# Performance work log

Measured on AMD Instinct MI355X. Metric: run time of the kernel, lower is better.

## Reference

```python
import jax, jax.numpy as jnp
import numpy as np

# Architecture constants (from init_kwargs)
IN_DIM, D_MODEL, HEADDIM, D_STATE, EXPAND, OUT_DIM = 57, 64, 32, 32, 2, 6
D_INNER = EXPAND * D_MODEL          # 128
NHEADS = D_INNER // HEADDIM         # 4
D_CONV = 4                          # causal depthwise conv width (mamba default)
D_XBC = D_INNER + 2 * D_STATE       # 192 (x, B, C share the conv)
D_IN_PROJ = 2 * D_INNER + 2 * D_STATE + NHEADS  # z, xBC, dt -> 324
BATCH, SEQ = 16, 2048


def setup_inputs() -> dict:
    key = jax.random.key(0)
    ks = jax.random.split(key, 12)
    s = 0.02
    return {
        "x": jax.random.normal(ks[0], (BATCH, SEQ, IN_DIM), jnp.float32),
        "W_lin": jax.random.normal(ks[1], (IN_DIM, D_MODEL), jnp.float32) * s,
        "b_lin": jnp.zeros((D_MODEL,), jnp.float32),
        "W_in": jax.random.normal(ks[2], (D_MODEL, D_IN_PROJ), jnp.float32) * s,
        "conv_w": jax.random.normal(ks[3], (D_XBC, 1, D_CONV), jnp.float32) * 0.5,
        "conv_b": jnp.zeros((D_XBC,), jnp.float32),
        "dt_bias": jnp.log(jax.random.uniform(ks[4], (NHEADS,), jnp.float32, 0.001, 0.1)),
        "A_log": jnp.log(jnp.arange(1, NHEADS + 1, dtype=jnp.float32)),
        "D": jnp.ones((NHEADS,), jnp.float32),
        "norm_w": jnp.ones((D_INNER,), jnp.float32),
        "W_out": jax.random.normal(ks[5], (D_INNER, D_MODEL), jnp.float32) * s,
        "W_cls": jax.random.normal(ks[6], (D_MODEL, OUT_DIM), jnp.float32) * s,
        "b_cls": jnp.zeros((OUT_DIM,), jnp.float32),
    }


def _mamba_block(h, W_in, conv_w, conv_b, dt_bias, A_log, D, norm_w, W_out):
    B, L, _ = h.shape
    zxbcdt = h @ W_in                                   # [B,L,324]
    z = zxbcdt[..., :D_INNER]                           # gate [B,L,128]
    xBC = zxbcdt[..., D_INNER:D_INNER + D_XBC]          # [B,L,192]
    dt = zxbcdt[..., D_INNER + D_XBC:]                  # [B,L,H]

    # causal depthwise conv over time + silu
    xBC = jax.lax.conv_general_dilated(
        xBC.transpose(0, 2, 1), conv_w, (1,), [(D_CONV - 1, 0)],
        dimension_numbers=("NCH", "OIH", "NCH"), feature_group_count=D_XBC)
    xBC = jax.nn.silu(xBC + conv_b[None, :, None]).transpose(0, 2, 1)

    xs = xBC[..., :D_INNER].reshape(B, L, NHEADS, HEADDIM)   # [B,L,H,P]
    Bm = xBC[..., D_INNER:D_INNER + D_STATE]                 # [B,L,N]
    Cm = xBC[..., D_INNER + D_STATE:]                        # [B,L,N]

    dt = jax.nn.softplus(dt + dt_bias)                       # [B,L,H]
    A = -jnp.exp(A_log)                                      # [H]

    def step(hstate, t):
        dtt, xt, bt, ct = t                                  # [B,H],[B,H,P],[B,N],[B,N]
        decay = jnp.exp(dtt * A)[:, :, None, None]           # [B,H,1,1]
        hstate = hstate * decay + (dtt[:, :, None] * xt)[..., None] * bt[:, None, None, :]
        y = jnp.einsum("bhpn,bn->bhp", hstate, ct)
        return hstate, y

    h0 = jnp.zeros((B, NHEADS, HEADDIM, D_STATE), h.dtype)
    _, ys = jax.lax.scan(step, h0, (dt.transpose(1, 0, 2), xs.transpose(1, 0, 2, 3),
                                    Bm.transpose(1, 0, 2), Cm.transpose(1, 0, 2)))
    y = ys.transpose(1, 0, 2, 3) + D[None, None, :, None] * xs   # [B,L,H,P]
    y = y.reshape(B, L, D_INNER)

    # gated RMSNorm + out proj
    y = y * jax.nn.silu(z)
    y = y * jax.lax.rsqrt(jnp.mean(y * y, axis=-1, keepdims=True) + 1e-5) * norm_w
    return y @ W_out                                        # [B,L,D_MODEL]


def reference(x, W_lin, b_lin, W_in, conv_w, conv_b, dt_bias, A_log, D, norm_w,
              W_out, W_cls, b_cls):
    h = x @ W_lin + b_lin                                   # linear_in
    h = _mamba_block(h, W_in, conv_w, conv_b, dt_bias, A_log, D, norm_w, W_out)
    pooled = h.mean(axis=1)                                 # AdaptiveAvgPool1d(1)
    return pooled @ W_cls + b_cls                           # classifier [B,6]
```

## Files before the change

kernel.cpp:

```cpp
#include <hip/hip_runtime.h>
#include <hip/hip_fp16.h>
#include <cmath>

#define BATCH   16
#define SEQ     2048
#define IN_DIM  57
#define D_MODEL 64
#define HEADDIM 32
#define D_STATE 32
#define OUT_DIM 6
#define D_INNER 128
#define NHEADS  4
#define D_CONV  4
#define D_XBC   192
#define D_IN_PROJ 324
#define BL      (BATCH*SEQ)

#define NCHUNK  64
#define CLEN    (SEQ / NCHUNK)
#define SUBL    16
#define XDS     200

#define OFF_WF   ((size_t)0)
#define OFF_BF   ((size_t)18496)
#define OFF_WOC  ((size_t)18848)
#define OFF_P    ((size_t)21792)
#define OFF_DC   ((size_t)25920)
#define OFF_ZB   ((size_t)157000)
#define OFF_CB   (OFF_ZB + (size_t)BL*64)
#define OFF_YB   (OFF_CB + (size_t)BL*16)
#define OFF_SB   (OFF_YB + (size_t)BL*64)

__global__ void fuse_w_kernel(const float* __restrict__ W_lin,
                              const float* __restrict__ b_lin,
                              const float* __restrict__ W_in,
                              const float* __restrict__ W_out,
                              const float* __restrict__ W_cls,
                              float* __restrict__ Wf, float* __restrict__ bf,
                              float* __restrict__ Woc,
                              const float* __restrict__ b_cls,
                              float* __restrict__ out) {
    int idx = blockIdx.x * 256 + threadIdx.x;
    if (idx < BATCH * OUT_DIM) out[idx] = b_cls[idx % OUT_DIM];
    if (idx < 58 * D_IN_PROJ) {
        int r = idx / D_IN_PROJ;
        int j = idx - r * D_IN_PROJ;
        const float* v = (r < IN_DIM) ? (W_lin + r * D_MODEL) : b_lin;
        float acc = 0.f;
#pragma unroll 8
        for (int m = 0; m < D_MODEL; ++m) acc += v[m] * W_in[m * D_IN_PROJ + j];
        if (r < IN_DIM) Wf[r * D_IN_PROJ + j] = acc;
        else            bf[j] = acc;
    } else if (idx < 58 * D_IN_PROJ + D_INNER * OUT_DIM) {
        int idx2 = idx - 58 * D_IN_PROJ;
        int i = idx2 / OUT_DIM;
        int o = idx2 - i * OUT_DIM;
        float acc = 0.f;
#pragma unroll 8
        for (int j = 0; j < D_MODEL; ++j)
            acc += W_out[i * D_MODEL + j] * W_cls[j * OUT_DIM + o];
        Woc[i * OUT_DIM + o] = acc;
    }
}

__global__ __launch_bounds__(256) void mega1_kernel(
        const float* __restrict__ x,
        const float* __restrict__ Wf, const float* __restrict__ bf,
        const float* __restrict__ conv_w, const float* __restrict__ conv_b,
        const float* __restrict__ dt_bias, const float* __restrict__ A_log,
        const float* __restrict__ Dp,
        __half* __restrict__ zbh,
        __half* __restrict__ sbuf, float* __restrict__ Pbuf,
        __half* __restrict__ ybuf, __half* __restrict__ Cbuf,
        float* __restrict__ Dcum) {
    __shared__ __align__(16) char smem[40112];
    float (*xs)[60]    = (float (*)[60])smem;
    float (*xbt)[D_XBC]= (float (*)[D_XBC])smem;
    __half (*xdl)[XDS] = (__half (*)[XDS])(smem + 24576);
    __half (*yl)[D_INNER] = (__half (*)[D_INNER])(smem + 24576);
    float (*ddl)[8]    = (float (*)[8])(smem + 38576);
    float* dcl         = (float*)(smem + 39600);

    int b = blockIdx.x >> 6;
    int c = blockIdx.x & (NCHUNK - 1);
    int tid = threadIdx.x;
    long rbase = (long)b * SEQ + (long)c * CLEN;

    for (int i = tid; i < 35 * IN_DIM; i += 256) {
        int r = i / IN_DIM, k = i - r * IN_DIM;
        float v = 0.f;
        if (c > 0 || r >= 3) v = x[(rbase - 3 + r) * IN_DIM + k];
        xs[r][k] = v;
    }
    __syncthreads();

    if (tid < 245) {
        int rset = tid / 49, cg = tid - rset * 49;
        int j0 = 128 + cg * 4;
        float4 bias = *(const float4*)(bf + j0);
        float4 acc[7];
#pragma unroll
        for (int r = 0; r < 7; ++r) acc[r] = bias;
        const float* w = Wf + j0;
        const float* xrow = &xs[rset * 7][0];
#pragma unroll 2
        for (int kc = 0; kc < 14; ++kc) {
            int k = kc * 4;
            float4 wv0 = *(const float4*)(w + (size_t)(k + 0) * D_IN_PROJ);
            float4 wv1 = *(const float4*)(w + (size_t)(k + 1) * D_IN_PROJ);
            float4 wv2 = *(const float4*)(w + (size_t)(k + 2) * D_IN_PROJ);
            float4 wv3 = *(const float4*)(w + (size_t)(k + 3) * D_IN_PROJ);
#pragma unroll
            for (int r = 0; r < 7; ++r) {
                float4 xv = *(const float4*)(xrow + r * 60 + k);
                acc[r].x += xv.x * wv0.x + xv.y * wv1.x + xv.z * wv2.x + xv.w * wv3.x;
                acc[r].y += xv.x * wv0.y + xv.y * wv1.y + xv.z * wv2.y + xv.w * wv3.y;
                acc[r].z += xv.x * wv0.z + xv.y * wv1.z + xv.z * wv2.z + xv.w * wv3.z;
                acc[r].w += xv.x * wv0.w + xv.y * wv1.w + xv.z * wv2.w + xv.w * wv3.w;
            }
        }
        {
            float4 wv = *(const float4*)(w + (size_t)56 * D_IN_PROJ);
#pragma unroll
            for (int r = 0; r < 7; ++r) {
                float xv = xrow[r * 60 + 56];
                acc[r].x += xv * wv.x; acc[r].y += xv * wv.y;
                acc[r].z += xv * wv.z; acc[r].w += xv * wv.w;
            }
        }
#pragma unroll
        for (int r = 0; r < 7; ++r) {
            int row = rset * 7 + r;
            *(__half2*)&xdl[row][j0 - 128]     = __floats2half2_rn(acc[r].x, acc[r].y);
            *(__half2*)&xdl[row][j0 - 128 + 2] = __floats2half2_rn(acc[r].z, acc[r].w);
        }
    }

    {
        int rset = tid >> 5, cg = tid & 31;
        int j0 = cg * 4;
        float4 bias = *(const float4*)(bf + j0);
        float4 acc[4];
#pragma unroll
        for (int r = 0; r < 4; ++r) acc[r] = bias;
        const float* w = Wf + j0;
        const float* xrow = &xs[3 + rset * 4][0];
#pragma unroll 2
        for (int kc = 0; kc < 14; ++kc) {
            int k = kc * 4;
            float4 wv0 = *(const float4*)(w + (size_t)(k + 0) * D_IN_PROJ);
            float4 wv1 = *(const float4*)(w + (size_t)(k + 1) * D_IN_PROJ);
            float4 wv2 = *(const float4*)(w + (size_t)(k + 2) * D_IN_PROJ);
            float4 wv3 = *(const float4*)(w + (size_t)(k + 3) * D_IN_PROJ);
#pragma unroll
            for (int r = 0; r < 4; ++r) {
                float4 xv = *(const float4*)(xrow + r * 60 + k);
                acc[r].x += xv.x * wv0.x + xv.y * wv1.x + xv.z * wv2.x + xv.w * wv3.x;
                acc[r].y += xv.x * wv0.y + xv.y * wv1.y + xv.z * wv2.y + xv.w * wv3.y;
                acc[r].z += xv.x * wv0.z + xv.y * wv1.z + xv.z * wv2.z + xv.w * wv3.z;
                acc[r].w += xv.x * wv0.w + xv.y * wv1.w + xv.z * wv2.w + xv.w * wv3.w;
            }
        }
        {
            float4 wv = *(const float4*)(w + (size_t)56 * D_IN_PROJ);
#pragma unroll
            for (int r = 0; r < 4; ++r) {
                float xv = xrow[r * 60 + 56];
                acc[r].x += xv * wv.x; acc[r].y += xv * wv.y;
                acc[r].z += xv * wv.z; acc[r].w += xv * wv.w;
            }
        }
#pragma unroll
        for (int r = 0; r < 4; ++r) {
            long row = rbase + rset * 4 + r;
            __half2 h01 = __floats2half2_rn(acc[r].x, acc[r].y);
            __half2 h23 = __floats2half2_rn(acc[r].z, acc[r].w);
            uint2 u;
            u.x = *(unsigned*)&h01;
            u.y = *(unsigned*)&h23;
            *(uint2*)(zbh + row * D_INNER + j0) = u;
        }
    }
    __syncthreads();

    if (tid < D_XBC) {
        int ch = tid;
        float w0 = conv_w[ch*4+0], w1 = conv_w[ch*4+1];
        float w2 = conv_w[ch*4+2], w3 = conv_w[ch*4+3];
        float cb = conv_b[ch];
        float vm1 = 0.f, vm2 = 0.f, vm3 = 0.f;
        if (c > 0) {
            vm1 = __half2float(xdl[2][ch]);
            vm2 = __half2float(xdl[1][ch]);
            vm3 = __half2float(xdl[0][ch]);
        }
#pragma unroll
        for (int i = 0; i < CLEN; ++i) {
            float v0 = __half2float(xdl[i + 3][ch]);
            float a = cb + v0 * w3 + vm1 * w2 + vm2 * w1 + vm3 * w0;
            xbt[i][ch] = a / (1.f + expf(-a));
            vm3 = vm2; vm2 = vm1; vm1 = v0;
        }
    } else {
        int idx = tid - D_XBC;
        int h = idx >> 4;
        int i0 = idx & 15;
        float db = dt_bias[h];
        float nA = -expf(A_log[h]);
#pragma unroll
        for (int i = i0; i < CLEN; i += 16) {
            float v = __half2float(xdl[i + 3][192 + h]) + db;
            float dtv = (v > 20.f) ? v : log1pf(expf(v));
            ddl[i][h * 2]     = dtv;
            ddl[i][h * 2 + 1] = expf(dtv * nA);
        }
    }
    __syncthreads();

    int h = tid >> 6, lane = tid & 63;
    int p = lane >> 1, n0 = (lane & 1) * 16;
    float Dh = Dp[h];
    float4 s0 = make_float4(0.f,0.f,0.f,0.f), s1 = s0, s2 = s0, s3 = s0;
    float pacc = 1.f;
#pragma unroll 4
    for (int i = 0; i < CLEN; ++i) {
        float dtv = ddl[i][h * 2];
        float dec = ddl[i][h * 2 + 1];
        float xv = xbt[i][h * HEADDIM + p];
        const float* Bp = &xbt[i][D_INNER + n0];
        const float* Cp = &xbt[i][D_INNER + D_STATE + n0];
        float4 B0 = *(const float4*)(Bp + 0);
        float4 B1 = *(const float4*)(Bp + 4);
        float4 B2 = *(const float4*)(Bp + 8);
        float4 B3 = *(const float4*)(Bp + 12);
        float4 C0 = *(const float4*)(Cp + 0);
        float4 C1 = *(const float4*)(Cp + 4);
        float4 C2 = *(const float4*)(Cp + 8);
        float4 C3 = *(const float4*)(Cp + 12);
        float coef = dtv * xv;
        s0.x = s0.x*dec + coef*B0.x; s0.y = s0.y*dec + coef*B0.y;
        s0.z = s0.z*dec + coef*B0.z; s0.w = s0.w*dec + coef*B0.w;
        s1.x = s1.x*dec + coef*B1.x; s1.y = s1.y*dec + coef*B1.y;
        s1.z = s1.z*dec + coef*B1.z; s1.w = s1.w*dec + coef*B1.w;
        s2.x = s2.x*dec + coef*B2.x; s2.y = s2.y*dec + coef*B2.y;
        s2.z = s2.z*dec + coef*B2.z; s2.w = s2.w*dec + coef*B2.w;
        s3.x = s3.x*dec + coef*B3.x; s3.y = s3.y*dec + coef*B3.y;
        s3.z = s3.z*dec + coef*B3.z; s3.w = s3.w*dec + coef*B3.w;
        pacc *= dec;
        float part = s0.x*C0.x + s0.y*C0.y + s0.z*C0.z + s0.w*C0.w
                   + s1.x*C1.x + s1.y*C1.y + s1.z*C1.z + s1.w*C1.w
                   + s2.x*C2.x + s2.y*C2.y + s2.z*C2.z + s2.w*C2.w
                   + s3.x*C3.x + s3.y*C3.y + s3.z*C3.z + s3.w*C3.w;
        part += __shfl_xor(part, 1);
        if (lane == 0) dcl[i * 4 + h] = pacc;
        if ((lane & 1) == 0)
            yl[i][h * HEADDIM + p] = __float2half(part + Dh * xv);
    }
    int bh = b * NHEADS + h;
    __half2 hs[8];
    hs[0] = __floats2half2_rn(s0.x, s0.y); hs[1] = __floats2half2_rn(s0.z, s0.w);
    hs[2] = __floats2half2_rn(s1.x, s1.y); hs[3] = __floats2half2_rn(s1.z, s1.w);
    hs[4] = __floats2half2_rn(s2.x, s2.y); hs[5] = __floats2half2_rn(s2.z, s2.w);
    hs[6] = __floats2half2_rn(s3.x, s3.y); hs[7] = __floats2half2_rn(s3.z, s3.w);
    uint4* sp = (uint4*)(sbuf + ((size_t)bh * NCHUNK + c) * 1024) + lane * 2;
    sp[0] = *(uint4*)&hs[0];
    sp[1] = *(uint4*)&hs[4];
    if (lane == 0) Pbuf[bh * NCHUNK + c] = pacc;
    __syncthreads();
    {
        const uint4* ysrc = (const uint4*)&yl[0][0];
        uint4* ydst = (uint4*)(ybuf + (size_t)rbase * D_INNER);
        ydst[tid]       = ysrc[tid];
        ydst[tid + 256] = ysrc[tid + 256];
    }
    for (int idx = tid; idx < CLEN * 16; idx += 256) {
        int r  = idx >> 4;
        int n2 = (idx & 15) * 2;
        __half2 hv = __floats2half2_rn(xbt[r][D_INNER + D_STATE + n2],
                                       xbt[r][D_INNER + D_STATE + n2 + 1]);
        *((__half2*)(Cbuf + ((size_t)rbase + r) * D_STATE + n2)) = hv;
    }
    if (tid < CLEN * 4) Dcum[(size_t)rbase * 4 + tid] = dcl[tid];
}

__global__ __launch_bounds__(256) void scan_phase2_kernel(
        __half* __restrict__ sbuf, const float* __restrict__ Pbuf) {
    __shared__ unsigned sl[NCHUNK][128];
    __shared__ float Pl[NCHUNK];
    int bh = blockIdx.x >> 2;
    int q  = blockIdx.x & 3;
    int tid = threadIdx.x;
    unsigned* s32 = (unsigned*)sbuf;
    size_t base = (size_t)bh * NCHUNK * 512 + (size_t)q * 128;
    if (tid < NCHUNK) Pl[tid] = Pbuf[bh * NCHUNK + tid];
    for (int k = tid; k < NCHUNK * 128; k += 256) {
        int c = k >> 7, j = k & 127;
        sl[c][j] = s32[base + (size_t)c * 512 + j];
    }
    __syncthreads();
    if (tid < 128) {
        float rx = 0.f, ry = 0.f;
        unsigned v = sl[0][tid];
#pragma unroll 8
        for (int c = 0; c < NCHUNK; ++c) {
            unsigned vn = (c + 1 < NCHUNK) ? sl[c + 1][tid] : 0u;
            float Pv = Pl[c];
            __half2 hv = *(__half2*)&v;
            float2 t = __half22float2(hv);
            __half2 hr = __floats2half2_rn(rx, ry);
            sl[c][tid] = *(unsigned*)&hr;
            rx = rx * Pv + t.x;
            ry = ry * Pv + t.y;
            v = vn;
        }
    }
    __syncthreads();
    for (int k = tid; k < NCHUNK * 128; k += 256) {
        int c = k >> 7, j = k & 127;
        s32[base + (size_t)c * 512 + j] = sl[c][j];
    }
}

__global__ __launch_bounds__(256) void scan_phase3_kernel(
        const __half* __restrict__ ybuf, const __half* __restrict__ Cbuf,
        const float* __restrict__ Dcum, const __half* __restrict__ zbh,
        const __half* __restrict__ sbuf, const float* __restrict__ norm_w,
        const float* __restrict__ Woc, float* __restrict__ out) {
    int b  = blockIdx.x >> 7;
    int sc = blockIdx.x & 127;
    int c  = sc >> 1;
    int tid = threadIdx.x;
    __shared__ float ylds[SUBL][D_INNER];
    __shared__ float dcl[SUBL * 4];
    __shared__ float red[4][D_INNER];
    __shared__ float snw[D_INNER];
    size_t rbase = (size_t)b * SEQ + (size_t)sc * SUBL;
    int h = tid >> 6, lane = tid & 63;
    int p = lane >> 1, n0 = (lane & 1) * 16;
    int bh = b * NHEADS + h;
    const uint4* sp = (const uint4*)(sbuf + ((size_t)bh * NCHUNK + c) * 1024) + lane * 2;
    uint4 u0 = sp[0], u1 = sp[1];
    {
        const __half2* ysrc = (const __half2*)(ybuf + rbase * D_INNER);
#pragma unroll
        for (int k = 0; k < 4; ++k) {
            int idx = tid + k * 256;
            float2 f = __half22float2(ysrc[idx]);
            int r  = idx >> 6;
            int c2 = (idx & 63) * 2;
            ylds[r][c2]     = f.x;
            ylds[r][c2 + 1] = f.y;
        }
    }
    if (tid < SUBL * 4) dcl[tid] = Dcum[rbase * 4 + tid];
    float4 s0, s1, s2, s3;
    {
        const __half2* hp0 = (const __half2*)&u0;
        const __half2* hp1 = (const __half2*)&u1;
        float2 f;
        f = __half22float2(hp0[0]); s0.x = f.x; s0.y = f.y;
        f = __half22float2(hp0[1]); s0.z = f.x; s0.w = f.y;
        f = __half22float2(hp0[2]); s1.x = f.x; s1.y = f.y;
        f = __half22float2(hp0[3]); s1.z = f.x; s1.w = f.y;
        f = __half22float2(hp1[0]); s2.x = f.x; s2.y = f.y;
        f = __half22float2(hp1[1]); s2.z = f.x; s2.w = f.y;
        f = __half22float2(hp1[2]); s3.x = f.x; s3.y = f.y;
        f = __half22float2(hp1[3]); s3.z = f.x; s3.w = f.y;
    }
    __syncthreads();
#pragma unroll 4
    for (int i = 0; i < SUBL; ++i) {
        const uint4* cp = (const uint4*)(Cbuf + (rbase + i) * D_STATE + n0);
        uint4 ca = cp[0], cb = cp[1];
        const __half2* cha = (const __half2*)&ca;
        const __half2* chb = (const __half2*)&cb;
        float2 f0 = __half22float2(cha[0]);
        float2 f1 = __half22float2(cha[1]);
        float2 f2 = __half22float2(cha[2]);
        float2 f3 = __half22float2(cha[3]);
        float2 f4 = __half22float2(chb[0]);
        float2 f5 = __half22float2(chb[1]);
        float2 f6 = __half22float2(chb[2]);
        float2 f7 = __half22float2(chb[3]);
        float part = s0.x*f0.x + s0.y*f0.y + s0.z*f1.x + s0.w*f1.y
                   + s1.x*f2.x + s1.y*f2.y + s1.z*f3.x + s1.w*f3.y
                   + s2.x*f4.x + s2.y*f4.y + s2.z*f5.x + s2.w*f5.y
                   + s3.x*f6.x + s3.y*f6.y + s3.z*f7.x + s3.w*f7.y;
        part += __shfl_xor(part, 1);
        if ((lane & 1) == 0)
            ylds[i][h * HEADDIM + p] += dcl[i * 4 + h] * part;
    }
    __syncthreads();
    float acc0 = 0.f, acc1 = 0.f;
    for (int r = h; r < SUBL; r += 4) {
        size_t bl = rbase + r;
        float2 yv = *(const float2*)(&ylds[r][lane * 2]);
        float2 zv = __half22float2(*((const __half2*)(zbh + bl * D_INNER) + lane));
        float g0 = yv.x * (zv.x / (1.f + expf(-zv.x)));
        float g1 = yv.y * (zv.y / (1.f + expf(-zv.y)));
        float sq = g0 * g0 + g1 * g1;
#pragma unroll
        for (int m = 1; m < 64; m <<= 1) sq += __shfl_xor(sq, m);
        float rms = 1.0f / sqrtf(sq * (1.f / 128.f) + 1e-5f);
        acc0 += g0 * rms;
        acc1 += g1 * rms;
    }
    red[h][lane * 2]     = acc0;
    red[h][lane * 2 + 1] = acc1;
    __syncthreads();
    if (tid < D_INNER)
        snw[tid] = (red[0][tid] + red[1][tid] + red[2][tid] + red[3][tid])
                   * norm_w[tid];
    __syncthreads();
    if (tid < OUT_DIM) {
        float acc = 0.f;
#pragma unroll 8
        for (int i = 0; i < D_INNER; ++i)
            acc += snw[i] * Woc[i * OUT_DIM + tid];
        atomicAdd(&out[b * OUT_DIM + tid], acc * (1.f / (float)SEQ));
    }
}

extern "C" void kernel_launch(void* const* d_in, const int* in_sizes, int n_in,
                              void* d_out, int out_size, void* d_ws, size_t ws_size,
                              hipStream_t stream) {
    const float* x       = (const float*)d_in[0];
    const float* W_lin   = (const float*)d_in[1];
    const float* b_lin   = (const float*)d_in[2];
    const float* W_in    = (const float*)d_in[3];
    const float* conv_w  = (const float*)d_in[4];
    const float* conv_b  = (const float*)d_in[5];
    const float* dt_bias = (const float*)d_in[6];
    const float* A_log   = (const float*)d_in[7];
    const float* Dp      = (const float*)d_in[8];
    const float* norm_w  = (const float*)d_in[9];
    const float* W_out   = (const float*)d_in[10];
    const float* W_cls   = (const float*)d_in[11];
    const float* b_cls   = (const float*)d_in[12];
    float* out = (float*)d_out;

    float* ws = (float*)d_ws;
    float* Wf    = ws + OFF_WF;
    float* bf    = ws + OFF_BF;
    float* Woc   = ws + OFF_WOC;
    float* Pbuf  = ws + OFF_P;
    float* Dcum  = ws + OFF_DC;
    __half* zbh  = (__half*)(ws + OFF_ZB);
    __half* Cbh  = (__half*)(ws + OFF_CB);
    __half* ybh  = (__half*)(ws + OFF_YB);
    __half* sbuf = (__half*)(ws + OFF_SB);

    fuse_w_kernel<<<(58 * D_IN_PROJ + D_INNER * OUT_DIM + 255) / 256, 256, 0, stream>>>(
        W_lin, b_lin, W_in, W_out, W_cls, Wf, bf, Woc, b_cls, out);

    mega1_kernel<<<BATCH * NCHUNK, 256, 0, stream>>>(
        x, Wf, bf, conv_w, conv_b, dt_bias, A_log, Dp,
        zbh, sbuf, Pbuf, ybh, Cbh, Dcum);

    scan_phase2_kernel<<<256, 256, 0, stream>>>(sbuf, Pbuf);

    scan_phase3_kernel<<<BATCH * 128, 256, 0, stream>>>(
        ybh, Cbh, Dcum, zbh, sbuf, norm_w, Woc, out);
}
```

Measured before the change: 168.1 us.

## Compute fused input projection with fp16 MFMA and pre-packed weights

Replaces the scalar FP32 fused linear_in+in_proj GEMM in the main kernel with MFMA 16x16x32 fp16 instructions. Weights are pre-packed in the prep kernel into an MFMA-friendly fp16 layout, and inputs are staged in LDS as XOR-swizzled fp16. The z-gate output now goes through LDS and is written out with coalesced 16-byte stores. This trades FP32 input precision for fp16 operands, which could affect accuracy.

Result: faster. 150.4 us (-10.6%).

```diff
diff --git a/kernel.cpp b/kernel.cpp
--- a/kernel.cpp
+++ b/kernel.cpp
@@ -21,12 +21,18 @@
 #define SUBL    16
 #define XDS     200
 
-#define OFF_WF   ((size_t)0)
-#define OFF_BF   ((size_t)18496)
-#define OFF_WOC  ((size_t)18848)
-#define OFF_P    ((size_t)21792)
-#define OFF_DC   ((size_t)25920)
-#define OFF_ZB   ((size_t)157000)
+#define NT      21
+#define WP_HALFS (NT * 2 * 64 * 8)
+
+typedef _Float16 f16x8 __attribute__((ext_vector_type(8)));
+typedef float    f32x4 __attribute__((ext_vector_type(4)));
+
+#define OFF_WP   ((size_t)0)
+#define OFF_BF   ((size_t)10752)
+#define OFF_WOC  ((size_t)11088)
+#define OFF_P    ((size_t)11856)
+#define OFF_DC   ((size_t)15952)
+#define OFF_ZB   ((size_t)147024)
 #define OFF_CB   (OFF_ZB + (size_t)BL*64)
 #define OFF_YB   (OFF_CB + (size_t)BL*16)
 #define OFF_SB   (OFF_YB + (size_t)BL*64)
@@ -36,23 +42,33 @@
                               const float* __restrict__ W_in,
                               const float* __restrict__ W_out,
                               const float* __restrict__ W_cls,
-                              float* __restrict__ Wf, float* __restrict__ bf,
+                              __half* __restrict__ Wph, float* __restrict__ bf,
                               float* __restrict__ Woc,
                               const float* __restrict__ b_cls,
                               float* __restrict__ out) {
     int idx = blockIdx.x * 256 + threadIdx.x;
-    if (idx < BATCH * OUT_DIM) out[idx] = b_cls[idx % OUT_DIM];
-    if (idx < 58 * D_IN_PROJ) {
-        int r = idx / D_IN_PROJ;
-        int j = idx - r * D_IN_PROJ;
-        const float* v = (r < IN_DIM) ? (W_lin + r * D_MODEL) : b_lin;
+    if (idx < 64 * 336) {
+        int k = idx / 336;
+        int n = idx - k * 336;
+        float acc = 0.f;
+        if (k < IN_DIM && n < D_IN_PROJ) {
+#pragma unroll 8
+            for (int m = 0; m < D_MODEL; ++m)
+                acc += W_lin[k * D_MODEL + m] * W_in[m * D_IN_PROJ + n];
+        }
+        int t = n >> 4, nl = n & 15;
+        int kb = k >> 5, kr = k & 31;
+        size_t pidx = (((size_t)(t * 2 + kb) * 64) + (kr >> 3) * 16 + nl) * 8 + (kr & 7);
+        Wph[pidx] = __float2half(acc);
+    } else if (idx < 64 * 336 + D_IN_PROJ) {
+        int n = idx - 64 * 336;
         float acc = 0.f;
 #pragma unroll 8
-        for (int m = 0; m < D_MODEL; ++m) acc += v[m] * W_in[m * D_IN_PROJ + j];
-        if (r < IN_DIM) Wf[r * D_IN_PROJ + j] = acc;
-        else            bf[j] = acc;
-    } else if (idx < 58 * D_IN_PROJ + D_INNER * OUT_DIM) {
-        int idx2 = idx - 58 * D_IN_PROJ;
+        for (int m = 0; m < D_MODEL; ++m)
+            acc += b_lin[m] * W_in[m * D_IN_PROJ + n];
+        bf[n] = acc;
+    } else if (idx < 64 * 336 + D_IN_PROJ + D_INNER * OUT_DIM) {
+        int idx2 = idx - (64 * 336 + D_IN_PROJ);
         int i = idx2 / OUT_DIM;
         int o = idx2 - i * OUT_DIM;
         float acc = 0.f;
@@ -60,12 +76,15 @@
         for (int j = 0; j < D_MODEL; ++j)
             acc += W_out[i * D_MODEL + j] * W_cls[j * OUT_DIM + o];
         Woc[i * OUT_DIM + o] = acc;
+    } else if (idx < 64 * 336 + D_IN_PROJ + D_INNER * OUT_DIM + BATCH * OUT_DIM) {
+        int idx3 = idx - (64 * 336 + D_IN_PROJ + D_INNER * OUT_DIM);
+        out[idx3] = b_cls[idx3 % OUT_DIM];
     }
 }
 
 __global__ __launch_bounds__(256) void mega1_kernel(
         const float* __restrict__ x,
-        const float* __restrict__ Wf, const float* __restrict__ bf,
+        const __half* __restrict__ Wph, const float* __restrict__ bf,
         const float* __restrict__ conv_w, const float* __restrict__ conv_b,
         const float* __restrict__ dt_bias, const float* __restrict__ A_log,
         const float* __restrict__ Dp,
@@ -74,7 +93,8 @@
         __half* __restrict__ ybuf, __half* __restrict__ Cbuf,
         float* __restrict__ Dcum) {
     __shared__ __align__(16) char smem[40112];
-    float (*xs)[60]    = (float (*)[60])smem;
+    __half* xsh        = (__half*)smem;
+    __half (*zl)[128]  = (__half (*)[128])(smem + 6144);
     float (*xbt)[D_XBC]= (float (*)[D_XBC])smem;
     __half (*xdl)[XDS] = (__half (*)[XDS])(smem + 24576);
     __half (*yl)[D_INNER] = (__half (*)[D_INNER])(smem + 24576);
@@ -86,100 +106,66 @@
     int tid = threadIdx.x;
     long rbase = (long)b * SEQ + (long)c * CLEN;
 
-    for (int i = tid; i < 35 * IN_DIM; i += 256) {
-        int r = i / IN_DIM, k = i - r * IN_DIM;
+    for (int i = tid; i < 48 * 64; i += 256) {
+        int r = i >> 6, k = i & 63;
         float v = 0.f;
-        if (c > 0 || r >= 3) v = x[(rbase - 3 + r) * IN_DIM + k];
-        xs[r][k] = v;
-    }
-    __syncthreads();
-
-    if (tid < 245) {
-        int rset = tid / 49, cg = tid - rset * 49;
-        int j0 = 128 + cg * 4;
-        float4 bias = *(const float4*)(bf + j0);
-        float4 acc[7];
-#pragma unroll
-        for (int r = 0; r < 7; ++r) acc[r] = bias;
-        const float* w = Wf + j0;
-        const float* xrow = &xs[rset * 7][0];
-#pragma unroll 2
-        for (int kc = 0; kc < 14; ++kc) {
-            int k = kc * 4;
-            float4 wv0 = *(const float4*)(w + (size_t)(k + 0) * D_IN_PROJ);
-            float4 wv1 = *(const float4*)(w + (size_t)(k + 1) * D_IN_PROJ);
-            float4 wv2 = *(const float4*)(w + (size_t)(k + 2) * D_IN_PROJ);
-            float4 wv3 = *(const float4*)(w + (size_t)(k + 3) * D_IN_PROJ);
-#pragma unroll
-            for (int r = 0; r < 7; ++r) {
-                float4 xv = *(const float4*)(xrow + r * 60 + k);
-                acc[r].x += xv.x * wv0.x + xv.y * wv1.x + xv.z * wv2.x + xv.w * wv3.x;
-                acc[r].y += xv.x * wv0.y + xv.y * wv1.y + xv.z * wv2.y + xv.w * wv3.y;
-                acc[r].z += xv.x * wv0.z + xv.y * wv1.z + xv.z * wv2.z + xv.w * wv3.z;
-                acc[r].w += xv.x * wv0.w + xv.y * wv1.w + xv.z * wv2.w + xv.w * wv3.w;
+        if (r < 35 && k < IN_DIM && (c > 0 || r >= 3))
+            v = x[(rbase - 3 + r) * IN_DIM + k];
+        xsh[i ^ ((r & 7) << 3)] = __float2half(v);
+    }
+    __syncthreads();
+
+    {
+        int wid = tid >> 6, lane = tid & 63;
+        int mrow = lane & 15, kg = lane >> 4;
+        union { uint4 u; f16x8 f; } a[3][2];
+#pragma unroll
+        for (int mt = 0; mt < 3; ++mt)
+#pragma unroll
+            for (int kb = 0; kb < 2; ++kb) {
+                int row = mt * 16 + mrow;
+                int hidx = (row * 64 + kb * 32 + kg * 8) ^ ((row & 7) << 3);
+                a[mt][kb].u = *(const uint4*)&xsh[hidx];
             }
-        }
-        {
-            float4 wv = *(const float4*)(w + (size_t)56 * D_IN_PROJ);
-#pragma unroll
-            for (int r = 0; r < 7; ++r) {
-                float xv = xrow[r * 60 + 56];
-                acc[r].x += xv * wv.x; acc[r].y += xv * wv.y;
-                acc[r].z += xv * wv.z; acc[r].w += xv * wv.w;
+        const uint4* wp4 = (const uint4*)Wph;
+        for (int t = wid; t < NT; t += 4) {
+            union { uint4 u; f16x8 f; } b0, b1;
+            b0.u = wp4[(t * 2 + 0) * 64 + lane];
+            b1.u = wp4[(t * 2 + 1) * 64 + lane];
+            float bias = bf[t * 16 + mrow];
+            f32x4 acc0 = {0.f, 0.f, 0.f, 0.f}, acc1 = acc0, acc2 = acc0;
+            acc0 = __builtin_amdgcn_mfma_f32_16x16x32_f16(a[0][0].f, b0.f, acc0, 0, 0, 0);
+            acc0 = __builtin_amdgcn_mfma_f32_16x16x32_f16(a[0][1].f, b1.f, acc0, 0, 0, 0);
+            acc1 = __builtin_amdgcn_mfma_f32_16x16x32_f16(a[1][0].f, b0.f, acc1, 0, 0, 0);
+            acc1 = __builtin_amdgcn_mfma_f32_16x16x32_f16(a[1][1].f, b1.f, acc1, 0, 0, 0);
+            acc2 = __builtin_amdgcn_mfma_f32_16x16x32_f16(a[2][0].f, b0.f, acc2, 0, 0, 0);
+            acc2 = __builtin_amdgcn_mfma_f32_16x16x32_f16(a[2][1].f, b1.f, acc2, 0, 0, 0);
+            int n = t * 16 + mrow;
+#pragma unroll
+            for (int mt = 0; mt < 3; ++mt) {
+                f32x4 av = (mt == 0) ? acc0 : (mt == 1) ? acc1 : acc2;
+#pragma unroll
+                for (int reg = 0; reg < 4; ++reg) {
+                    int m = mt * 16 + kg * 4 + reg;
+                    float v = av[reg] + bias;
+                    if (t < 8) {
+                        int zr = m - 3;
+                        if (zr >= 0 && zr < 32) zl[zr][n] = __float2half(v);
+                    } else {
+                        int xc = n - 128;
+                        if (m < 35 && xc < 196) xdl[m][xc] = __float2half(v);
+                    }
+                }
             }
         }
-#pragma unroll
-        for (int r = 0; r < 7; ++r) {
-            int row = rset * 7 + r;
-            *(__half2*)&xdl[row][j0 - 128]     = __floats2half2_rn(acc[r].x, acc[r].y);
-            *(__half2*)&xdl[row][j0 - 128 + 2] = __floats2half2_rn(acc[r].z, acc[r].w);
-        }
-    }
+    }
+    __syncthreads();
 
     {
-        int rset = tid >> 5, cg = tid & 31;
-        int j0 = cg * 4;
-        float4 bias = *(const float4*)(bf + j0);
-        float4 acc[4];
-#pragma unroll
-        for (int r = 0; r < 4; ++r) acc[r] = bias;
-        const float* w = Wf + j0;
-        const float* xrow = &xs[3 + rset * 4][0];
-#pragma unroll 2
-        for (int kc = 0; kc < 14; ++kc) {
-            int k = kc * 4;
-            float4 wv0 = *(const float4*)(w + (size_t)(k + 0) * D_IN_PROJ);
-            float4 wv1 = *(const float4*)(w + (size_t)(k + 1) * D_IN_PROJ);
-            float4 wv2 = *(const float4*)(w + (size_t)(k + 2) * D_IN_PROJ);
-            float4 wv3 = *(const float4*)(w + (size_t)(k + 3) * D_IN_PROJ);
-#pragma unroll
-            for (int r = 0; r < 4; ++r) {
-                float4 xv = *(const float4*)(xrow + r * 60 + k);
-                acc[r].x += xv.x * wv0.x + xv.y * wv1.x + xv.z * wv2.x + xv.w * wv3.x;
-                acc[r].y += xv.x * wv0.y + xv.y * wv1.y + xv.z * wv2.y + xv.w * wv3.y;
-                acc[r].z += xv.x * wv0.z + xv.y * wv1.z + xv.z * wv2.z + xv.w * wv3.z;
-                acc[r].w += xv.x * wv0.w + xv.y * wv1.w + xv.z * wv2.w + xv.w * wv3.w;
-            }
-        }
-        {
-            float4 wv = *(const float4*)(w + (size_t)56 * D_IN_PROJ);
-#pragma unroll
-            for (int r = 0; r < 4; ++r) {
-                float xv = xrow[r * 60 + 56];
-                acc[r].x += xv * wv.x; acc[r].y += xv * wv.y;
-                acc[r].z += xv * wv.z; acc[r].w += xv * wv.w;
-            }
-        }
-#pragma unroll
-        for (int r = 0; r < 4; ++r) {
-            long row = rbase + rset * 4 + r;
-            __half2 h01 = __floats2half2_rn(acc[r].x, acc[r].y);
-            __half2 h23 = __floats2half2_rn(acc[r].z, acc[r].w);
-            uint2 u;
-            u.x = *(unsigned*)&h01;
-            u.y = *(unsigned*)&h23;
-            *(uint2*)(zbh + row * D_INNER + j0) = u;
-        }
+        const uint4* zsrc = (const uint4*)&zl[0][0];
+        uint4* zdst = (uint4*)(zbh + (size_t)rbase * D_INNER);
+        zdst[tid]       = zsrc[tid];
+        zdst[tid + 256] = zsrc[tid + 256];
     }
     __syncthreads();
 
@@ -440,7 +426,7 @@
     float* out = (float*)d_out;
 
     float* ws = (float*)d_ws;
-    float* Wf    = ws + OFF_WF;
+    __half* Wph  = (__half*)(ws + OFF_WP);
     float* bf    = ws + OFF_BF;
     float* Woc   = ws + OFF_WOC;
     float* Pbuf  = ws + OFF_P;
@@ -450,11 +436,12 @@
     __half* ybh  = (__half*)(ws + OFF_YB);
     __half* sbuf = (__half*)(ws + OFF_SB);
 
-    fuse_w_kernel<<<(58 * D_IN_PROJ + D_INNER * OUT_DIM + 255) / 256, 256, 0, stream>>>(
-        W_lin, b_lin, W_in, W_out, W_cls, Wf, bf, Woc, b_cls, out);
+    int nfw = 64 * 336 + D_IN_PROJ + D_INNER * OUT_DIM + BATCH * OUT_DIM;
+    fuse_w_kernel<<<(nfw + 255) / 256, 256, 0, stream>>>(
+        W_lin, b_lin, W_in, W_out, W_cls, Wph, bf, Woc, b_cls, out);
 
     mega1_kernel<<<BATCH * NCHUNK, 256, 0, stream>>>(
-        x, Wf, bf, conv_w, conv_b, dt_bias, A_log, Dp,
+        x, Wph, bf, conv_w, conv_b, dt_bias, A_log, Dp,
         zbh, sbuf, Pbuf, ybh, Cbh, Dcum);
 
     scan_phase2_kernel<<<256, 256, 0, stream>>>(sbuf, Pbuf);
```
